# Performance work log

Measured on AMD Instinct MI355X. Metric: run time of the kernel, lower is better.

Reference implementation:

```python
import jax, jax.numpy as jnp
import numpy as np

N = 100000
E = 800000
D_IN = 512
D_OUT = 512
EPS = 1e-5


def setup_inputs() -> dict:
    key = jax.random.key(0)
    k = jax.random.split(key, 7)
    x = jax.random.normal(k[0], (N, D_IN), dtype=jnp.float32)
    edge_index = jax.random.randint(k[1], (2, E), 0, N, dtype=jnp.int64)
    # PyG SAGEConv params: lin_l (applied to aggregated neighbors, has bias), lin_r (root weight, no bias)
    W_l = jax.random.normal(k[2], (D_OUT, D_IN), dtype=jnp.float32) * 0.02
    b_l = jnp.zeros((D_OUT,), dtype=jnp.float32)
    W_r = jax.random.normal(k[3], (D_OUT, D_IN), dtype=jnp.float32) * 0.02
    # BatchNorm1d affine params (track_running_stats=False -> always batch stats)
    gamma = jnp.ones((D_OUT,), dtype=jnp.float32)
    beta = jnp.zeros((D_OUT,), dtype=jnp.float32)
    return {"x": x, "edge_index": edge_index, "W_l": W_l, "b_l": b_l,
            "W_r": W_r, "gamma": gamma, "beta": beta}


def reference(x, edge_index, W_l, b_l, W_r, gamma, beta):
    n = x.shape[0]
    src, dst = edge_index[0], edge_index[1]
    # mean-aggregate neighbor features: for each dst node, mean of x[src]
    summed = jax.ops.segment_sum(x[src], dst, num_segments=n)          # [N, D_IN]
    cnt = jax.ops.segment_sum(jnp.ones((src.shape[0],), x.dtype), dst, num_segments=n)
    aggr = summed / jnp.maximum(cnt, 1.0)[:, None]                      # zero-degree -> 0
    # SAGEConv: lin_l(aggr) + lin_r(x)
    h = aggr @ W_l.T + b_l + x @ W_r.T                                  # [N, D_OUT]
    # BatchNorm1d with batch statistics (biased variance), then ReLU
    mu = jnp.mean(h, axis=0)
    var = jnp.mean(jnp.square(h - mu), axis=0)
    h_norm = (h - mu) * jax.lax.rsqrt(var + EPS) * gamma + beta
    return jax.nn.relu(h_norm)
```

## Files before the change

kernel.cpp:

```cpp
#include <hip/hip_runtime.h>
#include <stdint.h>

#define D 512
#define K_TOT 1024
#define EPS 1e-5f
#define CHUNK 1024

typedef __bf16 bf16;
typedef bf16 bf16x4 __attribute__((ext_vector_type(4)));
typedef bf16 bf16x8 __attribute__((ext_vector_type(8)));
typedef float f32x4 __attribute__((ext_vector_type(4)));

__global__ void k_prep(const float* __restrict__ x, bf16* __restrict__ xb,
                       int* __restrict__ cnt, int* __restrict__ cur, float* __restrict__ stat,
                       bf16* __restrict__ padX, bf16* __restrict__ padA,
                       const float* __restrict__ Wl, const float* __restrict__ Wr,
                       bf16* __restrict__ Wc,
                       int n, int padGroups, size_t total8) {
  int gid = blockIdx.x * blockDim.x + threadIdx.x;
  int stride = gridDim.x * blockDim.x;
  if (gid < n) { cnt[gid] = 0; cur[gid] = 0; }
  if (gid < 2 * D) stat[gid] = 0.f;
  if (gid < padGroups) {
    bf16x8 z = {};
    *(bf16x8*)&padX[(size_t)gid * 8] = z;
    *(bf16x8*)&padA[(size_t)gid * 8] = z;
  }
  for (int w = gid; w < D * K_TOT; w += stride) {
    int o = w >> 10, k = w & 1023;
    float v = (k < D) ? Wr[o * D + k] : Wl[o * D + (k - D)];
    Wc[w] = (bf16)v;
  }
  size_t i = (size_t)gid;
  size_t sstride = (size_t)stride;
  const f32x4* xv = (const f32x4*)x;
  for (; i < total8; i += sstride) {
    f32x4 a = __builtin_nontemporal_load(xv + i * 2);
    f32x4 b = __builtin_nontemporal_load(xv + i * 2 + 1);
    bf16x8 v = { (bf16)a[0], (bf16)a[1], (bf16)a[2], (bf16)a[3],
                 (bf16)b[0], (bf16)b[1], (bf16)b[2], (bf16)b[3] };
    *(bf16x8*)&xb[i * 8] = v;
  }
}

__global__ void k_degree(const int* __restrict__ dst, int* __restrict__ cnt, int E) {
  int i = blockIdx.x * blockDim.x + threadIdx.x;
  int stride = gridDim.x * blockDim.x;
  for (; i < E; i += stride) atomicAdd(&cnt[dst[i]], 1);
}

__global__ void k_blocksum(const int* __restrict__ cnt, int* __restrict__ bsum, int n) {
  __shared__ int red[4];
  int b = blockIdx.x;
  int base = b * CHUNK;
  int s = 0;
  for (int i = threadIdx.x; i < CHUNK; i += 256) {
    int idx = base + i;
    s += (idx < n) ? cnt[idx] : 0;
  }
#pragma unroll
  for (int o = 32; o > 0; o >>= 1) s += __shfl_down(s, o);
  if ((threadIdx.x & 63) == 0) red[threadIdx.x >> 6] = s;
  __syncthreads();
  if (threadIdx.x == 0) bsum[b] = red[0] + red[1] + red[2] + red[3];
}

__global__ void k_scanb(int* __restrict__ bsum, int* __restrict__ bbase, int nb,
                        int* __restrict__ off, int n, int E) {
  if (threadIdx.x == 0) {
    int run = 0;
    for (int i = 0; i < nb; ++i) { bbase[i] = run; run += bsum[i]; }
    off[n] = E;
  }
}

__global__ void k_offsets(const int* __restrict__ cnt, const int* __restrict__ bbase,
                          int* __restrict__ off, int n) {
  __shared__ int tsum[256];
  int b = blockIdx.x;
  int i0 = b * CHUNK + threadIdx.x * 4;
  int vals[4];
  int s = 0;
#pragma unroll
  for (int j = 0; j < 4; ++j) {
    int idx = i0 + j;
    vals[j] = (idx < n) ? cnt[idx] : 0;
    s += vals[j];
  }
  tsum[threadIdx.x] = s;
  __syncthreads();
  for (int d = 1; d < 256; d <<= 1) {
    int v = (threadIdx.x >= d) ? tsum[threadIdx.x - d] : 0;
    __syncthreads();
    tsum[threadIdx.x] += v;
    __syncthreads();
  }
  int excl = tsum[threadIdx.x] - s + bbase[b];
#pragma unroll
  for (int j = 0; j < 4; ++j) {
    int idx = i0 + j;
    if (idx < n) off[idx] = excl;
    excl += vals[j];
  }
}

__global__ void k_fill(const int* __restrict__ src, const int* __restrict__ dst,
                       const int* __restrict__ off, int* __restrict__ cur,
                       int* __restrict__ csr, int E) {
  int i = blockIdx.x * blockDim.x + threadIdx.x;
  int stride = gridDim.x * blockDim.x;
  for (; i < E; i += stride) {
    int d = dst[i];
    int pos = off[d] + atomicAdd(&cur[d], 1);
    csr[pos] = src[i];
  }
}

__device__ __forceinline__ void acc8(float* c, uint4 u) {
  c[0] += __uint_as_float(u.x << 16);
  c[1] += __uint_as_float(u.x & 0xffff0000u);
  c[2] += __uint_as_float(u.y << 16);
  c[3] += __uint_as_float(u.y & 0xffff0000u);
  c[4] += __uint_as_float(u.z << 16);
  c[5] += __uint_as_float(u.z & 0xffff0000u);
  c[6] += __uint_as_float(u.w << 16);
  c[7] += __uint_as_float(u.w & 0xffff0000u);
}

__global__ __launch_bounds__(256) void k_gather(const bf16* __restrict__ xb,
                                                const int* __restrict__ off,
                                                const int* __restrict__ csr,
                                                bf16* __restrict__ aggr, int n) {
  int node = blockIdx.x * 4 + (threadIdx.x >> 6);
  if (node >= n) return;
  int lane = threadIdx.x & 63;
  int s0 = off[node], s1 = off[node + 1];
  float c[8] = {0.f, 0.f, 0.f, 0.f, 0.f, 0.f, 0.f, 0.f};
  int j = s0;
  for (; j + 7 < s1; j += 8) {
    int i0 = csr[j], i1 = csr[j + 1], i2 = csr[j + 2], i3 = csr[j + 3];
    int i4 = csr[j + 4], i5 = csr[j + 5], i6 = csr[j + 6], i7 = csr[j + 7];
    uint4 u0 = *((const uint4*)(xb + (size_t)i0 * D) + lane);
    uint4 u1 = *((const uint4*)(xb + (size_t)i1 * D) + lane);
    uint4 u2 = *((const uint4*)(xb + (size_t)i2 * D) + lane);
    uint4 u3 = *((const uint4*)(xb + (size_t)i3 * D) + lane);
    uint4 u4 = *((const uint4*)(xb + (size_t)i4 * D) + lane);
    uint4 u5 = *((const uint4*)(xb + (size_t)i5 * D) + lane);
    uint4 u6 = *((const uint4*)(xb + (size_t)i6 * D) + lane);
    uint4 u7 = *((const uint4*)(xb + (size_t)i7 * D) + lane);
    acc8(c, u0); acc8(c, u1); acc8(c, u2); acc8(c, u3);
    acc8(c, u4); acc8(c, u5); acc8(c, u6); acc8(c, u7);
  }
  for (; j + 3 < s1; j += 4) {
    int i0 = csr[j], i1 = csr[j + 1], i2 = csr[j + 2], i3 = csr[j + 3];
    uint4 u0 = *((const uint4*)(xb + (size_t)i0 * D) + lane);
    uint4 u1 = *((const uint4*)(xb + (size_t)i1 * D) + lane);
    uint4 u2 = *((const uint4*)(xb + (size_t)i2 * D) + lane);
    uint4 u3 = *((const uint4*)(xb + (size_t)i3 * D) + lane);
    acc8(c, u0); acc8(c, u1); acc8(c, u2); acc8(c, u3);
  }
  for (; j < s1; ++j) {
    int a = csr[j];
    uint4 u = *((const uint4*)(xb + (size_t)a * D) + lane);
    acc8(c, u);
  }
  float rinv = (s1 > s0) ? 1.0f / (float)(s1 - s0) : 0.0f;
  bf16x8 out = { (bf16)(c[0] * rinv), (bf16)(c[1] * rinv), (bf16)(c[2] * rinv), (bf16)(c[3] * rinv),
                 (bf16)(c[4] * rinv), (bf16)(c[5] * rinv), (bf16)(c[6] * rinv), (bf16)(c[7] * rinv) };
  *(bf16x8*)&aggr[(size_t)node * D + lane * 8] = out;
}

__device__ __forceinline__ void gl_lds16(const bf16* g, bf16* l) {
  __builtin_amdgcn_global_load_lds((const __attribute__((address_space(1))) unsigned int*)g,
                                   (__attribute__((address_space(3))) unsigned int*)l, 16, 0, 0);
}

template <int MREP, bool HB>
__global__ __launch_bounds__(512, 2) void k_gemm(const bf16* __restrict__ Xb,
                                                 const bf16* __restrict__ Aggr,
                                                 const bf16* __restrict__ Wc,
                                                 const float* __restrict__ bias,
                                                 bf16* __restrict__ Hb,
                                                 float* __restrict__ Cf,
                                                 float* __restrict__ stat,
                                                 int Mbase, int M) {
  __shared__ __align__(16) bf16 sA0[32 * MREP * 64];
  __shared__ __align__(16) bf16 sB0[256 * 64];
  __shared__ __align__(16) bf16 sA1[32 * MREP * 64];
  __shared__ __align__(16) bf16 sB1[256 * 64];
  const int tid = threadIdx.x;
  const int lane = tid & 63;
  const int wid = tid >> 6;
  const int wm = wid >> 2;
  const int wn = wid & 3;
  const int fr = lane & 15;
  const int fq = lane >> 4;

  const int bx = blockIdx.x >> 1;
  const int by = blockIdx.x & 1;
  const size_t rowA0 = (size_t)Mbase + (size_t)bx * (32 * MREP);
  const int rowB0 = by * 256;

  const int lrow = tid >> 3;
  const int scol = (((tid & 7) ^ (lrow & 7)) * 8);
  const bf16* pA_x = Xb + (rowA0 + lrow) * D + scol;
  const bf16* pA_g = Aggr + (rowA0 + lrow) * D + scol;
  const bf16* pB = Wc + (size_t)(rowB0 + lrow) * K_TOT + scol;
  bf16* ldsA0 = &sA0[lrow * 64 + (tid & 7) * 8];
  bf16* ldsB0 = &sB0[lrow * 64 + (tid & 7) * 8];
  bf16* ldsA1 = &sA1[lrow * 64 + (tid & 7) * 8];
  bf16* ldsB1 = &sB1[lrow * 64 + (tid & 7) * 8];

  f32x4 acc[MREP][4] = {};

#define STAGE(t, la, lb) do {                                                   \
    const bf16* As = ((t) < 8) ? pA_x : pA_g;                                   \
    const int ko = ((t) & 7) * 64;                                              \
    _Pragma("unroll")                                                           \
    for (int i = 0; i < MREP / 2; ++i)                                          \
      gl_lds16(As + (size_t)i * 64 * D + ko, (la) + i * 64 * 64);               \
    _Pragma("unroll")                                                           \
    for (int i = 0; i < 4; ++i)                                                 \
      gl_lds16(pB + (size_t)i * 64 * K_TOT + (t) * 64, (lb) + i * 64 * 64);     \
  } while (0)

#define COMPUTE(sa, sb) do {                                                    \
    _Pragma("unroll")                                                           \
    for (int kk = 0; kk < 2; ++kk) {                                            \
      const int cx = ((kk * 4 + fq) ^ (fr & 7)) * 8;                            \
      bf16x8 aF[MREP], bF[4];                                                   \
      _Pragma("unroll")                                                         \
      for (int m = 0; m < MREP; ++m)                                            \
        aF[m] = *(const bf16x8*)&(sa)[(wm * (16 * MREP) + m * 16 + fr) * 64 + cx]; \
      _Pragma("unroll")                                                         \
      for (int nn = 0; nn < 4; ++nn)                                            \
        bF[nn] = *(const bf16x8*)&(sb)[(wn * 64 + nn * 16 + fr) * 64 + cx];     \
      _Pragma("unroll")                                                         \
      for (int m = 0; m < MREP; ++m)                                            \
        _Pragma("unroll")                                                       \
        for (int nn = 0; nn < 4; ++nn)                                          \
          acc[m][nn] = __builtin_amdgcn_mfma_f32_16x16x32_bf16(aF[m], bF[nn], acc[m][nn], 0, 0, 0); \
    }                                                                           \
  } while (0)

  STAGE(0, ldsA0, ldsB0);
  __syncthreads();
#pragma unroll 1
  for (int t = 0; t < 16; t += 2) {
    STAGE(t + 1, ldsA1, ldsB1);
    COMPUTE(sA0, sB0);
    __syncthreads();
    if (t + 2 < 16) STAGE(t + 2, ldsA0, ldsB0);
    COMPUTE(sA1, sB1);
    __syncthreads();
  }
#undef STAGE
#undef COMPUTE

  const int rowb = (int)rowA0 + wm * (16 * MREP);
  const int colb = rowB0 + wn * 64;
  float s[4] = {0.f, 0.f, 0.f, 0.f}, q[4] = {0.f, 0.f, 0.f, 0.f};
#pragma unroll
  for (int nn = 0; nn < 4; ++nn) {
    int col = colb + nn * 16 + fr;
    float bv = bias[col];
#pragma unroll
    for (int m = 0; m < MREP; ++m) {
      int row0 = rowb + m * 16 + fq * 4;
#pragma unroll
      for (int r = 0; r < 4; ++r) {
        int row = row0 + r;
        if (row < M) {
          float v = acc[m][nn][r] + bv;
          if (HB) Hb[(size_t)row * D + col] = (bf16)v;
          else    Cf[(size_t)row * D + col] = v;
          s[nn] += v;
          q[nn] += v * v;
        }
      }
    }
  }
#pragma unroll
  for (int nn = 0; nn < 4; ++nn) {
    float sv = s[nn], qv = q[nn];
    sv += __shfl_down(sv, 32); sv += __shfl_down(sv, 16);
    qv += __shfl_down(qv, 32); qv += __shfl_down(qv, 16);
    if (lane < 16) {
      int col = colb + nn * 16 + fr;
      atomicAdd(&stat[col], sv);
      atomicAdd(&stat[D + col], qv);
    }
  }
}

template <bool HB>
__global__ void k_apply(const bf16* __restrict__ hb, const float* __restrict__ hf,
                        const float* __restrict__ stat, const float* __restrict__ gamma,
                        const float* __restrict__ beta, float* __restrict__ out,
                        int n, float invn) {
  size_t i = (size_t)blockIdx.x * blockDim.x + threadIdx.x;
  size_t stride = (size_t)gridDim.x * blockDim.x;
  size_t total = (size_t)n * (D / 4);
  f32x4* ov = (f32x4*)out;
  for (; i < total; i += stride) {
    int c4 = ((int)i & 127) * 4;
    float vx, vy, vz, vw;
    if (HB) {
      bf16x4 hv = *(const bf16x4*)&hb[i * 4];
      vx = (float)hv[0]; vy = (float)hv[1]; vz = (float)hv[2]; vw = (float)hv[3];
    } else {
      f32x4 v = ((const f32x4*)hf)[i];
      vx = v[0]; vy = v[1]; vz = v[2]; vw = v[3];
    }
    float4 st = *(const float4*)&stat[c4];
    float4 sq = *(const float4*)&stat[D + c4];
    float4 gm = *(const float4*)&gamma[c4];
    float4 bt = *(const float4*)&beta[c4];
    f32x4 o;
    {
      float mu = st.x * invn, var = sq.x * invn - mu * mu;
      float sc = gm.x * rsqrtf(var + EPS);
      o[0] = fmaxf(vx * sc + (bt.x - mu * sc), 0.f);
    }
    {
      float mu = st.y * invn, var = sq.y * invn - mu * mu;
      float sc = gm.y * rsqrtf(var + EPS);
      o[1] = fmaxf(vy * sc + (bt.y - mu * sc), 0.f);
    }
    {
      float mu = st.z * invn, var = sq.z * invn - mu * mu;
      float sc = gm.z * rsqrtf(var + EPS);
      o[2] = fmaxf(vz * sc + (bt.z - mu * sc), 0.f);
    }
    {
      float mu = st.w * invn, var = sq.w * invn - mu * mu;
      float sc = gm.w * rsqrtf(var + EPS);
      o[3] = fmaxf(vw * sc + (bt.w - mu * sc), 0.f);
    }
    __builtin_nontemporal_store(o, ov + i);
  }
}

extern "C" void kernel_launch(void* const* d_in, const int* in_sizes, int n_in,
                              void* d_out, int out_size, void* d_ws, size_t ws_size,
                              hipStream_t stream) {
  const float* x = (const float*)d_in[0];
  const int* ei = (const int*)d_in[1];
  const float* Wl = (const float*)d_in[2];
  const float* bl = (const float*)d_in[3];
  const float* Wr = (const float*)d_in[4];
  const float* gamma = (const float*)d_in[5];
  const float* beta = (const float*)d_in[6];
  float* out = (float*)d_out;

  const int E = in_sizes[1] / 2;
  const int n = in_sizes[0] / D;
  const int Mpad = ((n + 255) / 256) * 256;
  const int nb = (n + CHUNK - 1) / CHUNK;

  char* ws = (char*)d_ws;
  size_t off_b = 0;
  bf16* Xb   = (bf16*)(ws + off_b); off_b += (size_t)Mpad * D * sizeof(bf16);
  bf16* Aggr = (bf16*)(ws + off_b); off_b += (size_t)Mpad * D * sizeof(bf16);
  bf16* Wc   = (bf16*)(ws + off_b); off_b += (size_t)D * K_TOT * sizeof(bf16);
  int* cnt   = (int*)(ws + off_b);  off_b += (size_t)n * sizeof(int);
  int* offs  = (int*)(ws + off_b);  off_b += (size_t)(n + 1) * sizeof(int);
  int* cur   = (int*)(ws + off_b);  off_b += (size_t)n * sizeof(int);
  int* csr   = (int*)(ws + off_b);  off_b += (size_t)E * sizeof(int);
  int* bsum  = (int*)(ws + off_b);  off_b += 512 * sizeof(int);
  int* bbase = (int*)(ws + off_b);  off_b += 512 * sizeof(int);
  float* stat = (float*)(ws + off_b); off_b += 2 * D * sizeof(float);
  bf16* Hb   = (bf16*)(ws + off_b);
  const size_t need_hb = off_b + (size_t)Mpad * D * sizeof(bf16);
  const bool use_hb = (ws_size >= need_hb);

  const int* srcIdx = ei;
  const int* dstIdx = ei + E;
  const int padGroups = (Mpad - n) * D / 8;
  const float invn = 1.0f / (float)n;

  const int mb256 = Mpad / 256;
  int mainMB = (mb256 / 128) * 128;
  if (mainMB == 0) mainMB = mb256;
  const int tailMB = (Mpad - mainMB * 256) / 128;
  const int Mbase2 = mainMB * 256;

  k_prep<<<2048, 256, 0, stream>>>(x, Xb, cnt, cur, stat,
                                   Xb + (size_t)n * D, Aggr + (size_t)n * D,
                                   Wl, Wr, Wc,
                                   n, padGroups, (size_t)n * D / 8);
  k_degree<<<1024, 256, 0, stream>>>(dstIdx, cnt, E);
  k_blocksum<<<nb, 256, 0, stream>>>(cnt, bsum, n);
  k_scanb<<<1, 64, 0, stream>>>(bsum, bbase, nb, offs, n, E);
  k_offsets<<<nb, 256, 0, stream>>>(cnt, bbase, offs, n);
  k_fill<<<1024, 256, 0, stream>>>(srcIdx, dstIdx, offs, cur, csr, E);
  k_gather<<<(n + 3) / 4, 256, 0, stream>>>(Xb, offs, csr, Aggr, n);
  if (use_hb) {
    k_gemm<8, true><<<mainMB * 2, 512, 0, stream>>>(Xb, Aggr, Wc, bl, Hb, out, stat, 0, n);
    if (tailMB)
      k_gemm<4, true><<<tailMB * 2, 512, 0, stream>>>(Xb, Aggr, Wc, bl, Hb, out, stat, Mbase2, n);
    k_apply<true><<<2048, 256, 0, stream>>>(Hb, out, stat, gamma, beta, out, n, invn);
  } else {
    k_gemm<8, false><<<mainMB * 2, 512, 0, stream>>>(Xb, Aggr, Wc, bl, Hb, out, stat, 0, n);
    if (tailMB)
      k_gemm<4, false><<<tailMB * 2, 512, 0, stream>>>(Xb, Aggr, Wc, bl, Hb, out, stat, Mbase2, n);
    k_apply<false><<<2048, 256, 0, stream>>>(Hb, out, stat, gamma, beta, out, n, invn);
  }
}
```

Baseline: 529.3 us.

## Fuse CSR construction kernels into one cooperative kernel with grid syncs

Replaces the five separate CSR build launches (degree count, block sums, serial scan, offsets, fill) and the counter zeroing with a single cooperative kernel of 256 blocks that uses grid.sync between phases. The aim is to remove per-launch overhead and small-kernel gaps on the critical path before the gather. The trade-off is fewer blocks for the atomic degree and fill passes and the cost of grid-wide barriers. The single 256-block grid also only covers nb scan chunks if nb <= 256, which holds for N=100000 with CHUNK 1024.

```diff
diff --git a/kernel.cpp b/kernel.cpp
--- a/kernel.cpp
+++ b/kernel.cpp
@@ -1,5 +1,8 @@
 #include <hip/hip_runtime.h>
+#include <hip/hip_cooperative_groups.h>
 #include <stdint.h>
+
+namespace cg = cooperative_groups;
 
 #define D 512
 #define K_TOT 1024
@@ -12,14 +15,13 @@
 typedef float f32x4 __attribute__((ext_vector_type(4)));
 
 __global__ void k_prep(const float* __restrict__ x, bf16* __restrict__ xb,
-                       int* __restrict__ cnt, int* __restrict__ cur, float* __restrict__ stat,
+                       float* __restrict__ stat,
                        bf16* __restrict__ padX, bf16* __restrict__ padA,
                        const float* __restrict__ Wl, const float* __restrict__ Wr,
                        bf16* __restrict__ Wc,
-                       int n, int padGroups, size_t total8) {
+                       int padGroups, size_t total8) {
   int gid = blockIdx.x * blockDim.x + threadIdx.x;
   int stride = gridDim.x * blockDim.x;
-  if (gid < n) { cnt[gid] = 0; cur[gid] = 0; }
   if (gid < 2 * D) stat[gid] = 0.f;
   if (gid < padGroups) {
     bf16x8 z = {};
@@ -43,75 +45,77 @@
   }
 }
 
-__global__ void k_degree(const int* __restrict__ dst, int* __restrict__ cnt, int E) {
-  int i = blockIdx.x * blockDim.x + threadIdx.x;
-  int stride = gridDim.x * blockDim.x;
-  for (; i < E; i += stride) atomicAdd(&cnt[dst[i]], 1);
-}
-
-__global__ void k_blocksum(const int* __restrict__ cnt, int* __restrict__ bsum, int n) {
+__global__ void k_csr(const int* __restrict__ src, const int* __restrict__ dst,
+                      int* __restrict__ cnt, int* __restrict__ cur,
+                      int* __restrict__ offs, int* __restrict__ csr,
+                      int* __restrict__ bsum, int* __restrict__ bbase,
+                      int n, int E, int nb) {
+  cg::grid_group grid = cg::this_grid();
+  const int gid = blockIdx.x * blockDim.x + threadIdx.x;
+  const int stride = gridDim.x * blockDim.x;
   __shared__ int red[4];
-  int b = blockIdx.x;
-  int base = b * CHUNK;
-  int s = 0;
-  for (int i = threadIdx.x; i < CHUNK; i += 256) {
-    int idx = base + i;
-    s += (idx < n) ? cnt[idx] : 0;
-  }
-#pragma unroll
-  for (int o = 32; o > 0; o >>= 1) s += __shfl_down(s, o);
-  if ((threadIdx.x & 63) == 0) red[threadIdx.x >> 6] = s;
-  __syncthreads();
-  if (threadIdx.x == 0) bsum[b] = red[0] + red[1] + red[2] + red[3];
-}
-
-__global__ void k_scanb(int* __restrict__ bsum, int* __restrict__ bbase, int nb,
-                        int* __restrict__ off, int n, int E) {
-  if (threadIdx.x == 0) {
+  __shared__ int tsum[256];
+
+  for (int i = gid; i < n; i += stride) { cnt[i] = 0; cur[i] = 0; }
+  grid.sync();
+
+  for (int i = gid; i < E; i += stride) atomicAdd(&cnt[dst[i]], 1);
+  grid.sync();
+
+  if ((int)blockIdx.x < nb) {
+    int base = blockIdx.x * CHUNK;
+    int s = 0;
+    for (int i = threadIdx.x; i < CHUNK; i += 256) {
+      int idx = base + i;
+      s += (idx < n) ? cnt[idx] : 0;
+    }
+#pragma unroll
+    for (int o = 32; o > 0; o >>= 1) s += __shfl_down(s, o);
+    if ((threadIdx.x & 63) == 0) red[threadIdx.x >> 6] = s;
+    __syncthreads();
+    if (threadIdx.x == 0) bsum[blockIdx.x] = red[0] + red[1] + red[2] + red[3];
+  }
+  grid.sync();
+
+  if (gid == 0) {
     int run = 0;
     for (int i = 0; i < nb; ++i) { bbase[i] = run; run += bsum[i]; }
-    off[n] = E;
-  }
-}
-
-__global__ void k_offsets(const int* __restrict__ cnt, const int* __restrict__ bbase,
-                          int* __restrict__ off, int n) {
-  __shared__ int tsum[256];
-  int b = blockIdx.x;
-  int i0 = b * CHUNK + threadIdx.x * 4;
-  int vals[4];
-  int s = 0;
-#pragma unroll
-  for (int j = 0; j < 4; ++j) {
-    int idx = i0 + j;
-    vals[j] = (idx < n) ? cnt[idx] : 0;
-    s += vals[j];
-  }
-  tsum[threadIdx.x] = s;
-  __syncthreads();
-  for (int d = 1; d < 256; d <<= 1) {
-    int v = (threadIdx.x >= d) ? tsum[threadIdx.x - d] : 0;
+    offs[n] = E;
+  }
+  grid.sync();
+
+  if ((int)blockIdx.x < nb) {
+    int b = blockIdx.x;
+    int i0 = b * CHUNK + threadIdx.x * 4;
+    int vals[4];
+    int s = 0;
+#pragma unroll
+    for (int j = 0; j < 4; ++j) {
+      int idx = i0 + j;
+      vals[j] = (idx < n) ? cnt[idx] : 0;
+      s += vals[j];
+    }
+    tsum[threadIdx.x] = s;
     __syncthreads();
-    tsum[threadIdx.x] += v;
-    __syncthreads();
-  }
-  int excl = tsum[threadIdx.x] - s + bbase[b];
-#pragma unroll
-  for (int j = 0; j < 4; ++j) {
-    int idx = i0 + j;
-    if (idx < n) off[idx] = excl;
-    excl += vals[j];
-  }
-}
-
-__global__ void k_fill(const int* __restrict__ src, const int* __restrict__ dst,
-                       const int* __restrict__ off, int* __restrict__ cur,
-                       int* __restrict__ csr, int E) {
-  int i = blockIdx.x * blockDim.x + threadIdx.x;
-  int stride = gridDim.x * blockDim.x;
-  for (; i < E; i += stride) {
+    for (int d = 1; d < 256; d <<= 1) {
+      int v = (threadIdx.x >= (unsigned)d) ? tsum[threadIdx.x - d] : 0;
+      __syncthreads();
+      tsum[threadIdx.x] += v;
+      __syncthreads();
+    }
+    int excl = tsum[threadIdx.x] - s + bbase[b];
+#pragma unroll
+    for (int j = 0; j < 4; ++j) {
+      int idx = i0 + j;
+      if (idx < n) offs[idx] = excl;
+      excl += vals[j];
+    }
+  }
+  grid.sync();
+
+  for (int i = gid; i < E; i += stride) {
     int d = dst[i];
-    int pos = off[d] + atomicAdd(&cur[d], 1);
+    int pos = offs[d] + atomicAdd(&cur[d], 1);
     csr[pos] = src[i];
   }
 }
@@ -385,15 +389,21 @@
   const int tailMB = (Mpad - mainMB * 256) / 128;
   const int Mbase2 = mainMB * 256;
 
-  k_prep<<<2048, 256, 0, stream>>>(x, Xb, cnt, cur, stat,
+  k_prep<<<2048, 256, 0, stream>>>(x, Xb, stat,
                                    Xb + (size_t)n * D, Aggr + (size_t)n * D,
                                    Wl, Wr, Wc,
-                                   n, padGroups, (size_t)n * D / 8);
-  k_degree<<<1024, 256, 0, stream>>>(dstIdx, cnt, E);
-  k_blocksum<<<nb, 256, 0, stream>>>(cnt, bsum, n);
-  k_scanb<<<1, 64, 0, stream>>>(bsum, bbase, nb, offs, n, E);
-  k_offsets<<<nb, 256, 0, stream>>>(cnt, bbase, offs, n);
-  k_fill<<<1024, 256, 0, stream>>>(srcIdx, dstIdx, offs, cur, csr, E);
+                                   padGroups, (size_t)n * D / 8);
+
+  {
+    const int* srcA = srcIdx;
+    const int* dstA = dstIdx;
+    int nA = n, EA = E, nbA = nb;
+    void* args[] = { (void*)&srcA, (void*)&dstA, (void*)&cnt, (void*)&cur,
+                     (void*)&offs, (void*)&csr, (void*)&bsum, (void*)&bbase,
+                     (void*)&nA, (void*)&EA, (void*)&nbA };
+    hipLaunchCooperativeKernel((const void*)k_csr, dim3(256), dim3(256), args, 0, stream);
+  }
+
   k_gather<<<(n + 3) / 4, 256, 0, stream>>>(Xb, offs, csr, Aggr, n);
   if (use_hb) {
     k_gemm<8, true><<<mainMB * 2, 512, 0, stream>>>(Xb, Aggr, Wc, bl, Hb, out, stat, 0, n);
```

Result: slower. 654.4 us (+23.6%).
